# Performance work log

Hardware: AMD Instinct MI355X
Metric: run time of the kernel (lower is better)

## Reference

```python
import jax, jax.numpy as jnp
import numpy as np

N = 262144   # faces = edges = vertices
E = 2000000  # connections per bipartite edge set
W = 32       # out_width


def _linear_block(x, w, b):
    # LinearBlock(in, out) with defaults -> Linear + LeakyReLU(0.01)
    return jax.nn.leaky_relu(x @ w + b)


def _bip_res_mr_conv(x_src, x_dst, e, w, b):
    # diffs = x_dst[e1] - x_src[e0]; scatter_max over dst; MLP(cat) residual
    diffs = x_dst[e[1]] - x_src[e[0]]                       # [E, W]
    maxes = jax.ops.segment_max(diffs, e[1], num_segments=x_dst.shape[0])
    # torch_scatter.scatter_max fills empty slots with 0
    maxes = jnp.where(jnp.isfinite(maxes), maxes, 0.0)
    h = _linear_block(jnp.concatenate([x_dst, maxes], axis=1), w, b)
    return x_dst + h


def setup_inputs() -> dict:
    key = jax.random.key(0)
    ks = jax.random.split(key, 16)
    inp = {
        "x_f": jax.random.normal(ks[0], (N, 4), dtype=jnp.float32),
        "x_e": jax.random.normal(ks[1], (N, 6), dtype=jnp.float32),
        "x_v": jax.random.normal(ks[2], (N, 3), dtype=jnp.float32),
        "e_fe": jax.random.randint(ks[3], (2, E), 0, N),
        "e_ev": jax.random.randint(ks[4], (2, E), 0, N),
        "e_ef": jax.random.randint(ks[5], (2, E), 0, N),
        "e_ve": jax.random.randint(ks[6], (2, E), 0, N),
    }
    def lin(k, cin, cout):
        s = 1.0 / np.sqrt(cin)
        kw, kb = jax.random.split(k)
        return (jax.random.uniform(kw, (cin, cout), minval=-s, maxval=s, dtype=jnp.float32),
                jax.random.uniform(kb, (cout,), minval=-s, maxval=s, dtype=jnp.float32))
    inp["wf"], inp["bf"] = lin(ks[7], 4, W)
    inp["we"], inp["be"] = lin(ks[8], 6, W)
    inp["wv"], inp["bv"] = lin(ks[9], 3, W)
    inp["w_f2e"], inp["b_f2e"] = lin(ks[10], 2 * W, W)
    inp["w_e2v"], inp["b_e2v"] = lin(ks[11], 2 * W, W)   # E2V conv
    return inp


def reference(x_f, x_e, x_v, e_fe, e_ev, e_ef, e_ve,
              wf, bf, we, be, wv, bv, w_f2e, b_f2e, w_e2v, b_e2v):
    x_f = _linear_block(x_f, wf, bf)
    x_e = _linear_block(x_e, we, be)
    x_v = _linear_block(x_v, wv, bv)
    # NB: original forward reuses self.F2E weights for three convs
    x_e = _bip_res_mr_conv(x_f, x_e, e_fe, w_f2e, b_f2e)
    x_v = _bip_res_mr_conv(x_e, x_v, e_ev, w_e2v, b_e2v)
    x_f = _bip_res_mr_conv(x_e, x_f, e_ef, w_f2e, b_f2e)
    x_e = _bip_res_mr_conv(x_v, x_e, e_ve, w_f2e, b_f2e)
    return (x_f, x_e, x_v)
```

## Files before the change

kernel.cpp:

```cpp
#include <hip/hip_runtime.h>
#include <hip/hip_fp16.h>
#include <math.h>

#define N_NODES 262144
#define NE      2000000
#define W_OUT   32

#define NBINS          4096
#define BIN_SHIFT      6
#define NODES_PER_BIN  64
#define CAP            640
#define MROW           33
#define MXU_DW         ((((NODES_PER_BIN + 1) * MROW) + 3) & ~3)

__device__ __forceinline__ float lrelu(float x) { return x >= 0.f ? x : 0.01f * x; }

__device__ __forceinline__ unsigned fmin_key(float f) {
    unsigned u = __float_as_uint(f);
    return (u & 0x80000000u) ? ~u : (u | 0x80000000u);
}
__device__ __forceinline__ float fmin_unkey(unsigned u) {
    return __uint_as_float((u & 0x80000000u) ? (u ^ 0x80000000u) : ~u);
}

template<int K>
__global__ void proj_kernel(const float* __restrict__ x, const float* __restrict__ w,
                            const float* __restrict__ b, float* __restrict__ out,
                            __half* __restrict__ out_h) {
    __shared__ float wl[K * 32];
    __shared__ float xl[8 * K];
    int t = threadIdx.x;
    for (int i = t; i < K * 32; i += 256) wl[i] = w[i];
    int nbase = blockIdx.x * 8;
    for (int i = t; i < 8 * K; i += 256) xl[i] = x[nbase * K + i];
    __syncthreads();
    int j = t & 31, ln = t >> 5;
    float acc = b[j];
#pragma unroll
    for (int k = 0; k < K; ++k) acc += xl[ln * K + k] * wl[k * 32 + j];
    float r = lrelu(acc);
    out[nbase * 32 + t] = r;
    if (out_h) out_h[nbase * 32 + t] = __float2half(r);
}

__global__ __launch_bounds__(512)
void bin_pass4(const int* __restrict__ e0, const int* __restrict__ e1,
               int* __restrict__ gcur, unsigned int* __restrict__ buckets) {
    __shared__ unsigned int hist[NBINS];
    __shared__ unsigned int lcur[NBINS];
    __shared__ unsigned int gbase[NBINS];
    int t = threadIdx.x;
    for (int i = t; i < NBINS; i += 512) hist[i] = 0;
    __syncthreads();

    int q0 = blockIdx.x * 2048 + t;
    int4 d4[4];
#pragma unroll
    for (int k = 0; k < 4; ++k) {
        int q = q0 + k * 512;
        if (q < NE / 4) {
            d4[k] = ((const int4*)e1)[q];
            atomicAdd(&hist[((unsigned)d4[k].x) >> BIN_SHIFT], 1u);
            atomicAdd(&hist[((unsigned)d4[k].y) >> BIN_SHIFT], 1u);
            atomicAdd(&hist[((unsigned)d4[k].z) >> BIN_SHIFT], 1u);
            atomicAdd(&hist[((unsigned)d4[k].w) >> BIN_SHIFT], 1u);
        }
    }
    __syncthreads();
    for (int i = t; i < NBINS; i += 512) {
        unsigned h = hist[i];
        lcur[i] = 0;
        if (h) gbase[i] = atomicAdd((unsigned int*)&gcur[i], h);
    }
    __syncthreads();
#pragma unroll
    for (int k = 0; k < 4; ++k) {
        int q = q0 + k * 512;
        if (q < NE / 4) {
            int4 s4 = ((const int4*)e0)[q];
            const int ds[4] = {d4[k].x, d4[k].y, d4[k].z, d4[k].w};
            const int ss[4] = {s4.x, s4.y, s4.z, s4.w};
#pragma unroll
            for (int j = 0; j < 4; ++j) {
                unsigned d = (unsigned)ds[j];
                unsigned bin = d >> BIN_SHIFT;
                unsigned pos = gbase[bin] + atomicAdd(&lcur[bin], 1u);
                if (pos < CAP)
                    buckets[(size_t)bin * CAP + pos] =
                        ((d & (NODES_PER_BIN - 1u)) << 18) | (unsigned)ss[j];
            }
        }
    }
}

template<bool H>
__global__ __launch_bounds__(256)
void binreduce7(const int* __restrict__ gcur, const unsigned int* __restrict__ buckets,
                const float* __restrict__ src, const __half* __restrict__ src_h,
                const float* __restrict__ dst,
                const float* __restrict__ w, const float* __restrict__ b,
                float* __restrict__ out, __half* __restrict__ out_h) {
    __shared__ unsigned int mxu[MXU_DW];
    __shared__ float wl[64 * 32];
    __shared__ __align__(16) float xmat[8][2][64];
    int t = threadIdx.x;
    int bin = blockIdx.x;
    int hw = t >> 5, c = t & 31;

    uint4* m4 = (uint4*)mxu;
    for (int i = t; i < MXU_DW / 4; i += 256)
        m4[i] = make_uint4(0xFFFFFFFFu, 0xFFFFFFFFu, 0xFFFFFFFFu, 0xFFFFFFFFu);
    for (int i = t; i < 64 * 32; i += 256) wl[i] = w[i];
    __syncthreads();

    int nb = min(gcur[bin], CAP);
    const unsigned int* bk = buckets + (size_t)bin * CAP;
    const unsigned SENT = (unsigned)NODES_PER_BIN << 18;
    for (int cbase = hw * 32; cbase < nb; cbase += 256) {
        int idx = cbase + c;
        unsigned ent = (idx < nb) ? bk[idx] : SENT;
#pragma unroll
        for (int k0 = 0; k0 < 32; k0 += 8) {
            float v[8];
            unsigned nd[8];
#pragma unroll
            for (int j = 0; j < 8; ++j) {
                unsigned e = __shfl(ent, k0 + j, 32);
                nd[j] = e >> 18;
                size_t off = (size_t)(e & 0x3FFFFu) * 32 + c;
                if (H) v[j] = __half2float(src_h[off]);
                else   v[j] = src[off];
            }
#pragma unroll
            for (int j = 0; j < 8; ++j)
                atomicMin(&mxu[nd[j] * MROW + c], fmin_key(v[j]));
        }
    }
    __syncthreads();

    float bc = b[c];
    size_t gb = (size_t)bin * NODES_PER_BIN;
    for (int grp = 0; grp < 4; ++grp) {
        int n0 = hw * 8 + grp * 2;
#pragma unroll
        for (int gg = 0; gg < 2; ++gg) {
            int node = n0 + gg;
            float dv = dst[(gb + node) * 32 + c];
            unsigned mu = mxu[node * MROW + c];
            float mx = (mu == 0xFFFFFFFFu) ? 0.0f : (dv - fmin_unkey(mu));
            xmat[hw][gg][c] = dv;
            xmat[hw][gg][32 + c] = mx;
        }
        __threadfence_block();

        float acc0 = bc, acc1 = bc;
#pragma unroll 4
        for (int k4 = 0; k4 < 16; ++k4) {
            float w0 = wl[(k4 * 4 + 0) * 32 + c];
            float w1 = wl[(k4 * 4 + 1) * 32 + c];
            float w2 = wl[(k4 * 4 + 2) * 32 + c];
            float w3 = wl[(k4 * 4 + 3) * 32 + c];
            float4 x0 = ((const float4*)xmat[hw][0])[k4];
            float4 x1 = ((const float4*)xmat[hw][1])[k4];
            acc0 += x0.x * w0 + x0.y * w1 + x0.z * w2 + x0.w * w3;
            acc1 += x1.x * w0 + x1.y * w1 + x1.z * w2 + x1.w * w3;
        }
        float r0 = xmat[hw][0][c] + lrelu(acc0);
        float r1 = xmat[hw][1][c] + lrelu(acc1);
        out[(gb + n0 + 0) * 32 + c] = r0;
        out[(gb + n0 + 1) * 32 + c] = r1;
        if (out_h) {
            out_h[(gb + n0 + 0) * 32 + c] = __float2half(r0);
            out_h[(gb + n0 + 1) * 32 + c] = __float2half(r1);
        }
        __threadfence_block();
    }
}

extern "C" void kernel_launch(void* const* d_in, const int* in_sizes, int n_in,
                              void* d_out, int out_size, void* d_ws, size_t ws_size,
                              hipStream_t stream) {
    const float* x_f  = (const float*)d_in[0];
    const float* x_e  = (const float*)d_in[1];
    const float* x_v  = (const float*)d_in[2];
    const int*   e_fe = (const int*)d_in[3];
    const int*   e_ev = (const int*)d_in[4];
    const int*   e_ef = (const int*)d_in[5];
    const int*   e_ve = (const int*)d_in[6];
    const float* wf    = (const float*)d_in[7];
    const float* bf    = (const float*)d_in[8];
    const float* we    = (const float*)d_in[9];
    const float* be    = (const float*)d_in[10];
    const float* wv    = (const float*)d_in[11];
    const float* bv    = (const float*)d_in[12];
    const float* w_f2e = (const float*)d_in[13];
    const float* b_f2e = (const float*)d_in[14];
    const float* w_e2v = (const float*)d_in[15];
    const float* b_e2v = (const float*)d_in[16];

    float* of = (float*)d_out;
    float* oe = of + (size_t)N_NODES * W_OUT;
    float* ov = oe + (size_t)N_NODES * W_OUT;

    const size_t NW = (size_t)N_NODES * W_OUT;

    float*        xe1     = (float*)d_ws;
    unsigned int* buckets = (unsigned int*)(xe1 + NW);
    int*          gcur4   = (int*)(buckets + (size_t)NBINS * CAP);
    __half*       SA      = (__half*)(gcur4 + 4 * NBINS);
    __half*       SB      = SA + NW;

    const size_t need = NW * 4 + (size_t)NBINS * CAP * 4 + 4 * NBINS * 4 + 2 * NW * 2;
    const bool useH = ws_size >= need;
    if (!useH) { SA = nullptr; SB = nullptr; }

    dim3 blk(256);
    const int bgrid = (NE / 4 + 2047) / 2048;

    hipMemsetAsync(gcur4, 0, 4 * NBINS * sizeof(int), stream);

    proj_kernel<4><<<N_NODES / 8, blk, 0, stream>>>(x_f, wf, bf, of, SA);
    proj_kernel<6><<<N_NODES / 8, blk, 0, stream>>>(x_e, we, be, oe, nullptr);
    proj_kernel<3><<<N_NODES / 8, blk, 0, stream>>>(x_v, wv, bv, ov, nullptr);

    int conv_id = 0;
    auto conv = [&](const float* src, const __half* src_h, const float* dstb,
                    const int* e, const float* w, const float* bias,
                    float* out, __half* out_h) {
        int* gcur = gcur4 + conv_id * NBINS;
        ++conv_id;
        bin_pass4<<<bgrid, dim3(512), 0, stream>>>(e, e + NE, gcur, buckets);
        if (src_h)
            binreduce7<true><<<NBINS, blk, 0, stream>>>(gcur, buckets, src, src_h,
                                                        dstb, w, bias, out, out_h);
        else
            binreduce7<false><<<NBINS, blk, 0, stream>>>(gcur, buckets, src, nullptr,
                                                         dstb, w, bias, out, out_h);
    };

    conv(of,  SA, oe, e_fe, w_f2e, b_f2e, xe1, SB);
    conv(xe1, SB, ov, e_ev, w_e2v, b_e2v, ov,  SA);
    conv(xe1, SB, of, e_ef, w_f2e, b_f2e, of,  nullptr);
    conv(ov,  SA, xe1, e_ve, w_f2e, b_f2e, oe, nullptr);
}
```

Baseline: 481.5 us.

## Replace shared-memory atomicMin reduction with per-bin counting sort and register min

Bins become 256 nodes wide (1024 bins, capacity 2304), and the reduce kernel counting-sorts each bin's edges by local destination in shared memory. Each thread then reduces a contiguous segment in registers, using packed fp16 min on half-precision sources or float2 fminf otherwise. This drops the per-element shared atomicMin and the ordered-key transforms, and stores weights as float4. The cost is a prefix scan and extra syncs per block, fewer and larger blocks, and serial per-node loops whose trip counts vary with node degree.

New measurement: 594.7 us. 23.5% more time.

```diff
diff --git a/kernel.cpp b/kernel.cpp
--- a/kernel.cpp
+++ b/kernel.cpp
@@ -6,22 +6,19 @@
 #define NE      2000000
 #define W_OUT   32
 
-#define NBINS          4096
-#define BIN_SHIFT      6
-#define NODES_PER_BIN  64
-#define CAP            640
-#define MROW           33
-#define MXU_DW         ((((NODES_PER_BIN + 1) * MROW) + 3) & ~3)
+#define NBINS          1024
+#define BIN_SHIFT      8
+#define NPB            256
+#define CAP            2304
 
 __device__ __forceinline__ float lrelu(float x) { return x >= 0.f ? x : 0.01f * x; }
 
-__device__ __forceinline__ unsigned fmin_key(float f) {
-    unsigned u = __float_as_uint(f);
-    return (u & 0x80000000u) ? ~u : (u | 0x80000000u);
-}
-__device__ __forceinline__ float fmin_unkey(unsigned u) {
-    return __uint_as_float((u & 0x80000000u) ? (u ^ 0x80000000u) : ~u);
-}
+__device__ __forceinline__ unsigned pk_min_f16(unsigned a, unsigned b) {
+    unsigned r;
+    asm volatile("v_pk_min_f16 %0, %1, %2" : "=v"(r) : "v"(a), "v"(b));
+    return r;
+}
+#define HALF2_INF 0x7C007C00u
 
 template<int K>
 __global__ void proj_kernel(const float* __restrict__ x, const float* __restrict__ w,
@@ -44,7 +41,7 @@
 }
 
 __global__ __launch_bounds__(512)
-void bin_pass4(const int* __restrict__ e0, const int* __restrict__ e1,
+void bin_pass5(const int* __restrict__ e0, const int* __restrict__ e1,
                int* __restrict__ gcur, unsigned int* __restrict__ buckets) {
     __shared__ unsigned int hist[NBINS];
     __shared__ unsigned int lcur[NBINS];
@@ -53,10 +50,10 @@
     for (int i = t; i < NBINS; i += 512) hist[i] = 0;
     __syncthreads();
 
-    int q0 = blockIdx.x * 2048 + t;
-    int4 d4[4];
-#pragma unroll
-    for (int k = 0; k < 4; ++k) {
+    int q0 = blockIdx.x * 4096 + t;
+    int4 d4[8];
+#pragma unroll
+    for (int k = 0; k < 8; ++k) {
         int q = q0 + k * 512;
         if (q < NE / 4) {
             d4[k] = ((const int4*)e1)[q];
@@ -68,13 +65,12 @@
     }
     __syncthreads();
     for (int i = t; i < NBINS; i += 512) {
-        unsigned h = hist[i];
         lcur[i] = 0;
-        if (h) gbase[i] = atomicAdd((unsigned int*)&gcur[i], h);
-    }
-    __syncthreads();
-#pragma unroll
-    for (int k = 0; k < 4; ++k) {
+        gbase[i] = atomicAdd((unsigned int*)&gcur[i], hist[i]);
+    }
+    __syncthreads();
+#pragma unroll
+    for (int k = 0; k < 8; ++k) {
         int q = q0 + k * 512;
         if (q < NE / 4) {
             int4 s4 = ((const int4*)e0)[q];
@@ -87,7 +83,7 @@
                 unsigned pos = gbase[bin] + atomicAdd(&lcur[bin], 1u);
                 if (pos < CAP)
                     buckets[(size_t)bin * CAP + pos] =
-                        ((d & (NODES_PER_BIN - 1u)) << 18) | (unsigned)ss[j];
+                        ((d & (NPB - 1u)) << 18) | (unsigned)ss[j];
             }
         }
     }
@@ -95,59 +91,106 @@
 
 template<bool H>
 __global__ __launch_bounds__(256)
-void binreduce7(const int* __restrict__ gcur, const unsigned int* __restrict__ buckets,
-                const float* __restrict__ src, const __half* __restrict__ src_h,
-                const float* __restrict__ dst,
+void binreduce8(const int* __restrict__ gcur, const unsigned int* __restrict__ buckets,
+                const void* __restrict__ srcv, const float* __restrict__ dst,
                 const float* __restrict__ w, const float* __restrict__ b,
                 float* __restrict__ out, __half* __restrict__ out_h) {
-    __shared__ unsigned int mxu[MXU_DW];
-    __shared__ float wl[64 * 32];
-    __shared__ __align__(16) float xmat[8][2][64];
+    constexpr int MSTR = H ? 17 : 33;
+    __shared__ __align__(16) unsigned pool[CAP];
+    __shared__ unsigned cnt[NPB];
+    __shared__ unsigned offs_l[NPB + 1];
+    __shared__ unsigned mn[NPB * MSTR];
+    __shared__ __align__(16) float4 wl4[16 * 32];
     int t = threadIdx.x;
     int bin = blockIdx.x;
-    int hw = t >> 5, c = t & 31;
-
-    uint4* m4 = (uint4*)mxu;
-    for (int i = t; i < MXU_DW / 4; i += 256)
-        m4[i] = make_uint4(0xFFFFFFFFu, 0xFFFFFFFFu, 0xFFFFFFFFu, 0xFFFFFFFFu);
-    for (int i = t; i < 64 * 32; i += 256) wl[i] = w[i];
+    unsigned* sorted = pool;
+
+    cnt[t] = 0;
+    for (int i = t; i < 512; i += 256) {
+        int k4 = i >> 5, c = i & 31;
+        wl4[i] = make_float4(w[(k4 * 4 + 0) * 32 + c], w[(k4 * 4 + 1) * 32 + c],
+                             w[(k4 * 4 + 2) * 32 + c], w[(k4 * 4 + 3) * 32 + c]);
+    }
     __syncthreads();
 
     int nb = min(gcur[bin], CAP);
     const unsigned int* bk = buckets + (size_t)bin * CAP;
-    const unsigned SENT = (unsigned)NODES_PER_BIN << 18;
-    for (int cbase = hw * 32; cbase < nb; cbase += 256) {
-        int idx = cbase + c;
-        unsigned ent = (idx < nb) ? bk[idx] : SENT;
-#pragma unroll
-        for (int k0 = 0; k0 < 32; k0 += 8) {
-            float v[8];
-            unsigned nd[8];
-#pragma unroll
-            for (int j = 0; j < 8; ++j) {
-                unsigned e = __shfl(ent, k0 + j, 32);
-                nd[j] = e >> 18;
-                size_t off = (size_t)(e & 0x3FFFFu) * 32 + c;
-                if (H) v[j] = __half2float(src_h[off]);
-                else   v[j] = src[off];
-            }
-#pragma unroll
-            for (int j = 0; j < 8; ++j)
-                atomicMin(&mxu[nd[j] * MROW + c], fmin_key(v[j]));
-        }
-    }
-    __syncthreads();
-
+    for (int i = t; i < nb; i += 256)
+        atomicAdd(&cnt[bk[i] >> 18], 1u);
+    __syncthreads();
+
+    unsigned v = cnt[t];
+    offs_l[t] = v;
+    __syncthreads();
+    for (int d = 1; d < 256; d <<= 1) {
+        unsigned x = (t >= d) ? offs_l[t - d] : 0u;
+        __syncthreads();
+        offs_l[t] += x;
+        __syncthreads();
+    }
+    unsigned inc = offs_l[t];
+    __syncthreads();
+    offs_l[t] = inc - v;
+    if (t == 255) offs_l[NPB] = inc;
+    cnt[t] = 0;
+    __syncthreads();
+
+    for (int i = t; i < nb; i += 256) {
+        unsigned p = bk[i];
+        unsigned dl = p >> 18;
+        unsigned pos = offs_l[dl] + atomicAdd(&cnt[dl], 1u);
+        sorted[pos] = p & 0x3FFFFu;
+    }
+    __syncthreads();
+
+    int q = t & 15, g = t >> 4;
+    if (H) {
+        const unsigned* s2 = (const unsigned*)srcv;
+        for (int n = g * 16; n < g * 16 + 16; ++n) {
+            unsigned beg = offs_l[n], end = offs_l[n + 1];
+            unsigned acc = HALF2_INF;
+            for (unsigned i = beg; i < end; ++i) {
+                unsigned s = sorted[i];
+                acc = pk_min_f16(acc, s2[(size_t)s * 16 + q]);
+            }
+            mn[n * MSTR + q] = acc;
+        }
+    } else {
+        const float2* sf = (const float2*)srcv;
+        for (int n = g * 16; n < g * 16 + 16; ++n) {
+            unsigned beg = offs_l[n], end = offs_l[n + 1];
+            float a0 = INFINITY, a1 = INFINITY;
+            for (unsigned i = beg; i < end; ++i) {
+                unsigned s = sorted[i];
+                float2 vv = sf[(size_t)s * 16 + q];
+                a0 = fminf(a0, vv.x);
+                a1 = fminf(a1, vv.y);
+            }
+            mn[n * MSTR + 2 * q]     = __float_as_uint(a0);
+            mn[n * MSTR + 2 * q + 1] = __float_as_uint(a1);
+        }
+    }
+    __syncthreads();
+
+    float (*xmat)[2][64] = (float (*)[2][64])pool;
+    int hw = t >> 5, c = t & 31;
     float bc = b[c];
-    size_t gb = (size_t)bin * NODES_PER_BIN;
-    for (int grp = 0; grp < 4; ++grp) {
-        int n0 = hw * 8 + grp * 2;
+    size_t gb = (size_t)bin * NPB;
+    for (int grp = 0; grp < 16; ++grp) {
+        int n0 = hw * 32 + grp * 2;
 #pragma unroll
         for (int gg = 0; gg < 2; ++gg) {
             int node = n0 + gg;
             float dv = dst[(gb + node) * 32 + c];
-            unsigned mu = mxu[node * MROW + c];
-            float mx = (mu == 0xFFFFFFFFu) ? 0.0f : (dv - fmin_unkey(mu));
+            float mv;
+            if (H) {
+                unsigned mu = mn[node * MSTR + (c >> 1)];
+                float2 f2 = __half22float2(*(const __half2*)&mu);
+                mv = (c & 1) ? f2.y : f2.x;
+            } else {
+                mv = __uint_as_float(mn[node * MSTR + c]);
+            }
+            float mx = (mv == INFINITY) ? 0.0f : (dv - mv);
             xmat[hw][gg][c] = dv;
             xmat[hw][gg][32 + c] = mx;
         }
@@ -156,14 +199,11 @@
         float acc0 = bc, acc1 = bc;
 #pragma unroll 4
         for (int k4 = 0; k4 < 16; ++k4) {
-            float w0 = wl[(k4 * 4 + 0) * 32 + c];
-            float w1 = wl[(k4 * 4 + 1) * 32 + c];
-            float w2 = wl[(k4 * 4 + 2) * 32 + c];
-            float w3 = wl[(k4 * 4 + 3) * 32 + c];
+            float4 wv = wl4[k4 * 32 + c];
             float4 x0 = ((const float4*)xmat[hw][0])[k4];
             float4 x1 = ((const float4*)xmat[hw][1])[k4];
-            acc0 += x0.x * w0 + x0.y * w1 + x0.z * w2 + x0.w * w3;
-            acc1 += x1.x * w0 + x1.y * w1 + x1.z * w2 + x1.w * w3;
+            acc0 += x0.x * wv.x + x0.y * wv.y + x0.z * wv.z + x0.w * wv.w;
+            acc1 += x1.x * wv.x + x1.y * wv.y + x1.z * wv.z + x1.w * wv.w;
         }
         float r0 = xmat[hw][0][c] + lrelu(acc0);
         float r1 = xmat[hw][1][c] + lrelu(acc1);
@@ -215,9 +255,9 @@
     if (!useH) { SA = nullptr; SB = nullptr; }
 
     dim3 blk(256);
-    const int bgrid = (NE / 4 + 2047) / 2048;
-
-    hipMemsetAsync(gcur4, 0, 4 * NBINS * sizeof(int), stream);
+    const int bgrid = (NE / 4 + 4095) / 4096;
+
+    (void)hipMemsetAsync(gcur4, 0, 4 * NBINS * sizeof(int), stream);
 
     proj_kernel<4><<<N_NODES / 8, blk, 0, stream>>>(x_f, wf, bf, of, SA);
     proj_kernel<6><<<N_NODES / 8, blk, 0, stream>>>(x_e, we, be, oe, nullptr);
@@ -229,12 +269,12 @@
                     float* out, __half* out_h) {
         int* gcur = gcur4 + conv_id * NBINS;
         ++conv_id;
-        bin_pass4<<<bgrid, dim3(512), 0, stream>>>(e, e + NE, gcur, buckets);
+        bin_pass5<<<bgrid, dim3(512), 0, stream>>>(e, e + NE, gcur, buckets);
         if (src_h)
-            binreduce7<true><<<NBINS, blk, 0, stream>>>(gcur, buckets, src, src_h,
+            binreduce8<true><<<NBINS, blk, 0, stream>>>(gcur, buckets, (const void*)src_h,
                                                         dstb, w, bias, out, out_h);
         else
-            binreduce7<false><<<NBINS, blk, 0, stream>>>(gcur, buckets, src, nullptr,
+            binreduce8<false><<<NBINS, blk, 0, stream>>>(gcur, buckets, (const void*)src,
                                                          dstb, w, bias, out, out_h);
     };
 
```

## Use 128-node bins, store fp16 order-preserving keys, and pack weights as float4

Applied to the files above, without the earlier changes.

Halves the number of destination bins to 2048, with 128 nodes and up to 1200 entries each, so every reduce block handles twice as many nodes and there are fewer launches' worth of blocks. Source features are now stored as precomputed 16-bit sortable keys instead of fp16 values, which removes per-element conversion and key computation before the shared-memory atomicMin. Weights are repacked into float4 in shared memory so each k4 step does one vector LDS instead of four scalar loads. The larger bins roughly double shared memory per block and may lower occupancy, and the fixed CAP of 1200 can silently drop edges if a bin overflows.

New measurement: 418.3 us. -13.1%, faster.

```diff
diff --git a/kernel.cpp b/kernel.cpp
--- a/kernel.cpp
+++ b/kernel.cpp
@@ -6,15 +6,23 @@
 #define NE      2000000
 #define W_OUT   32
 
-#define NBINS          4096
-#define BIN_SHIFT      6
-#define NODES_PER_BIN  64
-#define CAP            640
+#define NBINS          2048
+#define BIN_SHIFT      7
+#define NPB            128
+#define CAP            1200
 #define MROW           33
-#define MXU_DW         ((((NODES_PER_BIN + 1) * MROW) + 3) & ~3)
+#define MXU_DW         ((((NPB + 1) * MROW) + 3) & ~3)
 
 __device__ __forceinline__ float lrelu(float x) { return x >= 0.f ? x : 0.01f * x; }
 
+__device__ __forceinline__ unsigned short key16f(float r) {
+    unsigned short u = __half_as_ushort(__float2half(r));
+    return (u & 0x8000u) ? (unsigned short)(~u) : (unsigned short)(u | 0x8000u);
+}
+__device__ __forceinline__ float unkey16(unsigned k) {
+    unsigned bits = (k & 0x8000u) ? (k ^ 0x8000u) : ((~k) & 0xFFFFu);
+    return __half2float(__ushort_as_half((unsigned short)bits));
+}
 __device__ __forceinline__ unsigned fmin_key(float f) {
     unsigned u = __float_as_uint(f);
     return (u & 0x80000000u) ? ~u : (u | 0x80000000u);
@@ -26,7 +34,7 @@
 template<int K>
 __global__ void proj_kernel(const float* __restrict__ x, const float* __restrict__ w,
                             const float* __restrict__ b, float* __restrict__ out,
-                            __half* __restrict__ out_h) {
+                            unsigned short* __restrict__ out_k) {
     __shared__ float wl[K * 32];
     __shared__ float xl[8 * K];
     int t = threadIdx.x;
@@ -40,11 +48,11 @@
     for (int k = 0; k < K; ++k) acc += xl[ln * K + k] * wl[k * 32 + j];
     float r = lrelu(acc);
     out[nbase * 32 + t] = r;
-    if (out_h) out_h[nbase * 32 + t] = __float2half(r);
+    if (out_k) out_k[nbase * 32 + t] = key16f(r);
 }
 
 __global__ __launch_bounds__(512)
-void bin_pass4(const int* __restrict__ e0, const int* __restrict__ e1,
+void bin_pass3(const int* __restrict__ e0, const int* __restrict__ e1,
                int* __restrict__ gcur, unsigned int* __restrict__ buckets) {
     __shared__ unsigned int hist[NBINS];
     __shared__ unsigned int lcur[NBINS];
@@ -68,9 +76,8 @@
     }
     __syncthreads();
     for (int i = t; i < NBINS; i += 512) {
-        unsigned h = hist[i];
         lcur[i] = 0;
-        if (h) gbase[i] = atomicAdd((unsigned int*)&gcur[i], h);
+        if (hist[i]) gbase[i] = atomicAdd((unsigned int*)&gcur[i], hist[i]);
     }
     __syncthreads();
 #pragma unroll
@@ -87,7 +94,7 @@
                 unsigned pos = gbase[bin] + atomicAdd(&lcur[bin], 1u);
                 if (pos < CAP)
                     buckets[(size_t)bin * CAP + pos] =
-                        ((d & (NODES_PER_BIN - 1u)) << 18) | (unsigned)ss[j];
+                        ((d & (NPB - 1u)) << 18) | (unsigned)ss[j];
             }
         }
     }
@@ -95,13 +102,12 @@
 
 template<bool H>
 __global__ __launch_bounds__(256)
-void binreduce7(const int* __restrict__ gcur, const unsigned int* __restrict__ buckets,
-                const float* __restrict__ src, const __half* __restrict__ src_h,
-                const float* __restrict__ dst,
+void binreduce9(const int* __restrict__ gcur, const unsigned int* __restrict__ buckets,
+                const void* __restrict__ srcv, const float* __restrict__ dst,
                 const float* __restrict__ w, const float* __restrict__ b,
-                float* __restrict__ out, __half* __restrict__ out_h) {
-    __shared__ unsigned int mxu[MXU_DW];
-    __shared__ float wl[64 * 32];
+                float* __restrict__ out, unsigned short* __restrict__ out_k) {
+    __shared__ unsigned mxu[MXU_DW];
+    __shared__ __align__(16) float4 wl4[16 * 32];
     __shared__ __align__(16) float xmat[8][2][64];
     int t = threadIdx.x;
     int bin = blockIdx.x;
@@ -110,44 +116,51 @@
     uint4* m4 = (uint4*)mxu;
     for (int i = t; i < MXU_DW / 4; i += 256)
         m4[i] = make_uint4(0xFFFFFFFFu, 0xFFFFFFFFu, 0xFFFFFFFFu, 0xFFFFFFFFu);
-    for (int i = t; i < 64 * 32; i += 256) wl[i] = w[i];
+    for (int i = t; i < 512; i += 256) {
+        int k4 = i >> 5, cc = i & 31;
+        wl4[i] = make_float4(w[(k4 * 4 + 0) * 32 + cc], w[(k4 * 4 + 1) * 32 + cc],
+                             w[(k4 * 4 + 2) * 32 + cc], w[(k4 * 4 + 3) * 32 + cc]);
+    }
     __syncthreads();
 
     int nb = min(gcur[bin], CAP);
     const unsigned int* bk = buckets + (size_t)bin * CAP;
-    const unsigned SENT = (unsigned)NODES_PER_BIN << 18;
+    const unsigned SENT = (unsigned)NPB << 18;
+    const unsigned short* sk = (const unsigned short*)srcv;
+    const float* sf = (const float*)srcv;
     for (int cbase = hw * 32; cbase < nb; cbase += 256) {
         int idx = cbase + c;
         unsigned ent = (idx < nb) ? bk[idx] : SENT;
 #pragma unroll
         for (int k0 = 0; k0 < 32; k0 += 8) {
-            float v[8];
-            unsigned nd[8];
+            unsigned v[8], nd[8];
 #pragma unroll
             for (int j = 0; j < 8; ++j) {
                 unsigned e = __shfl(ent, k0 + j, 32);
                 nd[j] = e >> 18;
                 size_t off = (size_t)(e & 0x3FFFFu) * 32 + c;
-                if (H) v[j] = __half2float(src_h[off]);
-                else   v[j] = src[off];
+                if (H) v[j] = (unsigned)sk[off];
+                else   v[j] = fmin_key(sf[off]);
             }
 #pragma unroll
             for (int j = 0; j < 8; ++j)
-                atomicMin(&mxu[nd[j] * MROW + c], fmin_key(v[j]));
+                atomicMin(&mxu[nd[j] * MROW + c], v[j]);
         }
     }
     __syncthreads();
 
     float bc = b[c];
-    size_t gb = (size_t)bin * NODES_PER_BIN;
-    for (int grp = 0; grp < 4; ++grp) {
-        int n0 = hw * 8 + grp * 2;
+    size_t gb = (size_t)bin * NPB;
+    for (int grp = 0; grp < 8; ++grp) {
+        int n0 = hw * 16 + grp * 2;
 #pragma unroll
         for (int gg = 0; gg < 2; ++gg) {
             int node = n0 + gg;
             float dv = dst[(gb + node) * 32 + c];
             unsigned mu = mxu[node * MROW + c];
-            float mx = (mu == 0xFFFFFFFFu) ? 0.0f : (dv - fmin_unkey(mu));
+            float mx;
+            if (H) mx = (mu > 0xFFFFu) ? 0.0f : (dv - unkey16(mu));
+            else   mx = (mu == 0xFFFFFFFFu) ? 0.0f : (dv - fmin_unkey(mu));
             xmat[hw][gg][c] = dv;
             xmat[hw][gg][32 + c] = mx;
         }
@@ -156,22 +169,19 @@
         float acc0 = bc, acc1 = bc;
 #pragma unroll 4
         for (int k4 = 0; k4 < 16; ++k4) {
-            float w0 = wl[(k4 * 4 + 0) * 32 + c];
-            float w1 = wl[(k4 * 4 + 1) * 32 + c];
-            float w2 = wl[(k4 * 4 + 2) * 32 + c];
-            float w3 = wl[(k4 * 4 + 3) * 32 + c];
+            float4 wv = wl4[k4 * 32 + c];
             float4 x0 = ((const float4*)xmat[hw][0])[k4];
             float4 x1 = ((const float4*)xmat[hw][1])[k4];
-            acc0 += x0.x * w0 + x0.y * w1 + x0.z * w2 + x0.w * w3;
-            acc1 += x1.x * w0 + x1.y * w1 + x1.z * w2 + x1.w * w3;
+            acc0 += x0.x * wv.x + x0.y * wv.y + x0.z * wv.z + x0.w * wv.w;
+            acc1 += x1.x * wv.x + x1.y * wv.y + x1.z * wv.z + x1.w * wv.w;
         }
         float r0 = xmat[hw][0][c] + lrelu(acc0);
         float r1 = xmat[hw][1][c] + lrelu(acc1);
         out[(gb + n0 + 0) * 32 + c] = r0;
         out[(gb + n0 + 1) * 32 + c] = r1;
-        if (out_h) {
-            out_h[(gb + n0 + 0) * 32 + c] = __float2half(r0);
-            out_h[(gb + n0 + 1) * 32 + c] = __float2half(r1);
+        if (out_k) {
+            out_k[(gb + n0 + 0) * 32 + c] = key16f(r0);
+            out_k[(gb + n0 + 1) * 32 + c] = key16f(r1);
         }
         __threadfence_block();
     }
@@ -204,11 +214,11 @@
 
     const size_t NW = (size_t)N_NODES * W_OUT;
 
-    float*        xe1     = (float*)d_ws;
-    unsigned int* buckets = (unsigned int*)(xe1 + NW);
-    int*          gcur4   = (int*)(buckets + (size_t)NBINS * CAP);
-    __half*       SA      = (__half*)(gcur4 + 4 * NBINS);
-    __half*       SB      = SA + NW;
+    float*          xe1     = (float*)d_ws;
+    unsigned int*   buckets = (unsigned int*)(xe1 + NW);
+    int*            gcur4   = (int*)(buckets + (size_t)NBINS * CAP);
+    unsigned short* SA      = (unsigned short*)(gcur4 + 4 * NBINS);
+    unsigned short* SB      = SA + NW;
 
     const size_t need = NW * 4 + (size_t)NBINS * CAP * 4 + 4 * NBINS * 4 + 2 * NW * 2;
     const bool useH = ws_size >= need;
@@ -217,25 +227,25 @@
     dim3 blk(256);
     const int bgrid = (NE / 4 + 2047) / 2048;
 
-    hipMemsetAsync(gcur4, 0, 4 * NBINS * sizeof(int), stream);
+    (void)hipMemsetAsync(gcur4, 0, 4 * NBINS * sizeof(int), stream);
 
     proj_kernel<4><<<N_NODES / 8, blk, 0, stream>>>(x_f, wf, bf, of, SA);
     proj_kernel<6><<<N_NODES / 8, blk, 0, stream>>>(x_e, we, be, oe, nullptr);
     proj_kernel<3><<<N_NODES / 8, blk, 0, stream>>>(x_v, wv, bv, ov, nullptr);
 
     int conv_id = 0;
-    auto conv = [&](const float* src, const __half* src_h, const float* dstb,
+    auto conv = [&](const float* src, const unsigned short* src_k, const float* dstb,
                     const int* e, const float* w, const float* bias,
-                    float* out, __half* out_h) {
+                    float* out, unsigned short* out_k) {
         int* gcur = gcur4 + conv_id * NBINS;
         ++conv_id;
-        bin_pass4<<<bgrid, dim3(512), 0, stream>>>(e, e + NE, gcur, buckets);
-        if (src_h)
-            binreduce7<true><<<NBINS, blk, 0, stream>>>(gcur, buckets, src, src_h,
-                                                        dstb, w, bias, out, out_h);
+        bin_pass3<<<bgrid, dim3(512), 0, stream>>>(e, e + NE, gcur, buckets);
+        if (src_k)
+            binreduce9<true><<<NBINS, blk, 0, stream>>>(gcur, buckets, (const void*)src_k,
+                                                        dstb, w, bias, out, out_k);
         else
-            binreduce7<false><<<NBINS, blk, 0, stream>>>(gcur, buckets, src, nullptr,
-                                                         dstb, w, bias, out, out_h);
+            binreduce9<false><<<NBINS, blk, 0, stream>>>(gcur, buckets, (const void*)src,
+                                                         dstb, w, bias, out, out_k);
     };
 
     conv(of,  SA, oe, e_fe, w_f2e, b_f2e, xe1, SB);
```
